# Kernel tuning notes

Hardware: AMD Instinct MI355X
Metric: run time of the kernel (lower is better)

The kernel has to match this reference:

```python
import jax, jax.numpy as jnp
import numpy as np

_SQRT2 = 1.4142135623730951

def _norm_cdf(z):
    return 0.5 * (1.0 + jax.scipy.special.erf(z / _SQRT2))

def _cv_squared(v):
    # torch.var is unbiased (ddof=1)
    return jnp.var(v, ddof=1) / (jnp.mean(v) ** 2 + 1e-10)

def setup_inputs() -> dict:
    key = jax.random.key(0)
    ks = jax.random.split(key, 6)
    B, Cin, Cout, H, W, E = 64, 32, 32, 64, 64, 16
    return {
        "x": jax.random.normal(ks[0], (B, Cin, H, W), jnp.float32),
        "noise": jax.random.normal(ks[1], (B, E), jnp.float32),
        "w_gate": jax.random.normal(ks[2], (Cin, E), jnp.float32) * 0.1,
        "w_noise": jax.random.normal(ks[3], (Cin, E), jnp.float32) * 0.1,
        "expert_w": jax.random.normal(ks[4], (E, Cout, Cin, 3, 3), jnp.float32) * 0.05,
        "expert_b": jax.random.normal(ks[5], (E, Cout), jnp.float32) * 0.05,
    }

def _forward(x, noise, w_gate, w_noise, expert_w, expert_b, k=4, loss_coef=0.01, noise_eps=0.01):
    B = x.shape[0]
    # gate features: adaptive avg pool to 1x1 then flatten -> [B, Cin]
    gate_x = x.mean(axis=(2, 3))
    clean = gate_x @ w_gate                      # [B, E]
    std = jax.nn.softplus(gate_x @ w_noise) + noise_eps
    noisy = clean + noise * std                  # noisy logits (training path)
    logits = jax.nn.softmax(noisy, axis=1)       # NOTE: original softmaxes before top-k
    top_logits, top_idx = jax.lax.top_k(logits, k + 1)
    top_k_logits = top_logits[:, :k]
    top_k_idx = top_idx[:, :k]
    top_k_gates = top_k_logits / (top_k_logits.sum(1, keepdims=True) + 1e-6)
    gates = jnp.zeros_like(logits).at[jnp.arange(B)[:, None], top_k_idx].set(top_k_gates)
    # _prob_in_top_k: thresholds come from the post-softmax top values,
    # compared against pre-softmax clean/noisy logits (faithful to source)
    thr_in = top_logits[:, k:k + 1]
    thr_out = top_logits[:, k - 1:k]
    prob = jnp.where(noisy > thr_in,
                     _norm_cdf((clean - thr_in) / std),
                     _norm_cdf((clean - thr_out) / std))
    load = prob.sum(0)
    importance = gates.sum(0)
    loss = (_cv_squared(importance) + _cv_squared(load)) * loss_coef
    # dispatch/combine: since gates are exactly zero for unselected experts,
    # sum_e gates[:,e] * expert_e(x) equals SparseDispatcher's gather-compute-scatter.
    def step(acc, xs):
        w, b, g = xs  # w [Co,Ci,3,3], b [Co], g [B]
        out = jax.lax.conv_general_dilated(x, w, (1, 1), [(1, 1), (1, 1)])
        out = out + b[None, :, None, None]
        return acc + g[:, None, None, None] * out, None
    y0 = jnp.zeros((B, expert_w.shape[1], x.shape[2], x.shape[3]), x.dtype)
    y, _ = jax.lax.scan(step, y0, (expert_w, expert_b, gates.T))
    return y, loss

def reference(x, noise, w_gate, w_noise, expert_w, expert_b):
    return _forward(x, noise, w_gate, w_noise, expert_w, expert_b)
```

## Files before the change

kernel.cpp:

```cpp
#include <hip/hip_runtime.h>
#include <math.h>

#define B 64
#define CIN 32
#define COUT 32
#define E 16
#define TOPK 4

typedef __attribute__((ext_vector_type(8))) short short8;
typedef __attribute__((ext_vector_type(4))) float f32x4;

__device__ __forceinline__ unsigned short f2bf(float f) {
    unsigned int u = __float_as_uint(f);
    u += 0x7fffu + ((u >> 16) & 1u);
    return (unsigned short)(u >> 16);
}

__device__ __forceinline__ int swz1024(int o) { return (o & 7) * 128 + (o >> 3); }

__device__ __forceinline__ int cswz(int wp, int c) {
    return c ^ (((wp >> 2) & 3) << 3);
}

__global__ void __launch_bounds__(256)
bandsum_kernel(const float* __restrict__ x, float* __restrict__ bandsum) {
    int blk = swz1024(blockIdx.x);
    int b = blk >> 4, band = blk & 15, h0 = band << 2;
    int t = threadIdx.x, wave = t >> 6, l = t & 63;
    const float4* x4 = reinterpret_cast<const float4*>(x);

    float racc[8];
    #pragma unroll
    for (int k = 0; k < 8; k++) {
        int c = k * 4 + wave;
        float4 v = x4[(((size_t)(b * 32 + c) * 64 + h0 + (l >> 4)) << 4) + (l & 15)];
        racc[k] = (v.x + v.y) + (v.z + v.w);
    }
    #pragma unroll
    for (int off = 1; off < 64; off <<= 1)
        #pragma unroll
        for (int k = 0; k < 8; k++) racc[k] += __shfl_xor(racc[k], off, 64);
    if (l == 0) {
        #pragma unroll
        for (int k = 0; k < 8; k++)
            bandsum[((size_t)b * 16 + band) * 32 + k * 4 + wave] = racc[k];
    }
}

__global__ void __launch_bounds__(256)
conv_fused(const float* __restrict__ x,
           const float* __restrict__ bandsum,
           const float* __restrict__ noise,
           const float* __restrict__ w_gate,
           const float* __restrict__ w_noise,
           const float* __restrict__ expert_w,
           const float* __restrict__ expert_b,
           float* __restrict__ probw,
           float* __restrict__ gimpw,
           float* __restrict__ y) {
    int blk = swz1024(blockIdx.x);
    int b = blk >> 4, band = blk & 15, h0 = band << 2;
    int t = threadIdx.x, wave = t >> 6, l = t & 63;
    int ln = l & 15, lk = l >> 4;

    __shared__ unsigned short sx[6 * 66 * 32];
    __shared__ unsigned short cw[9 * 1024];
    __shared__ float gx[32], s_bias[32];
    __shared__ float s_clean[E], s_std[E], s_noisy[E], s_lg[E];
    __shared__ float s_tv[TOPK + 1], s_g[TOPK];
    __shared__ int   s_gi[TOPK];

    if (t < 32) {
        const float* bp = bandsum + (size_t)b * 16 * 32 + t;
        float s = 0.f;
        #pragma unroll
        for (int j = 0; j < 16; j++) s += bp[j * 32];
        gx[t] = s * (1.f / 4096.f);
    }
    __syncthreads();
    if (t < E) {
        float s1 = 0.f, s2 = 0.f;
        #pragma unroll
        for (int c = 0; c < CIN; c++) {
            float g = gx[c];
            s1 += g * w_gate[c * E + t];
            s2 += g * w_noise[c * E + t];
        }
        float sp = fmaxf(s2, 0.f) + log1pf(expf(-fabsf(s2)));
        s_clean[t] = s1;
        s_std[t]   = sp + 0.01f;
        s_noisy[t] = s1 + noise[b * E + t] * (sp + 0.01f);
    }
    __syncthreads();
    if (t < E) {
        float m = s_noisy[0];
        #pragma unroll
        for (int e = 1; e < E; e++) m = fmaxf(m, s_noisy[e]);
        float den = 0.f;
        #pragma unroll
        for (int e = 0; e < E; e++) den += expf(s_noisy[e] - m);
        s_lg[t] = expf(s_noisy[t] - m) / den;
    }
    __syncthreads();
    if (t < E) {
        float v = s_lg[t]; int rank = 0;
        #pragma unroll
        for (int j = 0; j < E; j++) {
            float u = s_lg[j];
            rank += (u > v) || (u == v && j < t);
        }
        if (rank <= TOPK) s_tv[rank] = v;
        if (rank <  TOPK) s_gi[rank] = t;
    }
    __syncthreads();
    if (t < TOPK) {
        float s4 = s_tv[0] + s_tv[1] + s_tv[2] + s_tv[3] + 1e-6f;
        s_g[t] = s_tv[t] / s4;
    }
    __syncthreads();

    if (band == 0 && t < E) {
        float s4 = s_tv[0] + s_tv[1] + s_tv[2] + s_tv[3] + 1e-6f;
        float v = s_lg[t]; int rank = 0;
        #pragma unroll
        for (int j = 0; j < E; j++) {
            float u = s_lg[j];
            rank += (u > v) || (u == v && j < t);
        }
        gimpw[b * E + t] = (rank < TOPK) ? v / s4 : 0.f;
        const float INV_SQRT2 = 0.70710678118654752f;
        float thr_in = s_tv[TOPK], thr_out = s_tv[TOPK - 1];
        float thr = (s_noisy[t] > thr_in) ? thr_in : thr_out;
        float z = (s_clean[t] - thr) / s_std[t];
        probw[b * E + t] = 0.5f * (1.f + erff(z * INV_SQRT2));
    }

    const float4* x4 = reinterpret_cast<const float4*>(x);
    #pragma unroll
    for (int k = 0; k < 12; k++) {
        int i = k * 256 + t;
        int rr = i >> 9, c = (i >> 4) & 31, w4 = i & 15;
        int gr = h0 - 1 + rr;
        float4 v = {0.f, 0.f, 0.f, 0.f};
        if ((unsigned)gr < 64u)
            v = x4[(((size_t)(b * 32 + c) * 64 + gr) << 4) + w4];
        float vv[4] = {v.x, v.y, v.z, v.w};
        #pragma unroll
        for (int j = 0; j < 4; j++) {
            int wp = 1 + w4 * 4 + j;
            sx[(rr * 66 + wp) * 32 + cswz(wp, c)] = f2bf(vv[j]);
        }
    }
    for (int i = t; i < 384; i += 256) {
        int rr = i >> 6, rem = i & 63, side = rem >> 5, c = rem & 31;
        sx[(rr * 66 + side * 65) * 32 + c] = 0;
    }
    {
        const float* e0 = expert_w + s_gi[0] * 9216;
        const float* e1 = expert_w + s_gi[1] * 9216;
        const float* e2 = expert_w + s_gi[2] * 9216;
        const float* e3 = expert_w + s_gi[3] * 9216;
        float g0 = s_g[0], g1 = s_g[1], g2 = s_g[2], g3 = s_g[3];
        #pragma unroll
        for (int k = 0; k < 36; k++) {
            int o = k * 256 + t;
            int cc = o / 9, tap = o - cc * 9;
            float s = g0 * e0[o] + g1 * e1[o] + g2 * e2[o] + g3 * e3[o];
            cw[tap * 1024 + cc] = f2bf(s);
        }
        if (t < 32)
            s_bias[t] = g0 * expert_b[s_gi[0] * 32 + t] + g1 * expert_b[s_gi[1] * 32 + t]
                      + g2 * expert_b[s_gi[2] * 32 + t] + g3 * expert_b[s_gi[3] * 32 + t];
    }
    __syncthreads();

    short8 afrag[2][9];
    #pragma unroll
    for (int tap = 0; tap < 9; tap++)
        #pragma unroll
        for (int ch = 0; ch < 2; ch++)
            afrag[ch][tap] = *reinterpret_cast<const short8*>(
                &cw[tap * 1024 + (ch * 16 + ln) * 32 + lk * 8]);

    float bias0[4], bias1[4];
    #pragma unroll
    for (int r = 0; r < 4; r++) {
        bias0[r] = s_bias[lk * 4 + r];
        bias1[r] = s_bias[16 + lk * 4 + r];
    }

    int h = h0 + wave;
    for (int tile = 0; tile < 4; tile++) {
        int w0 = tile * 16;
        f32x4 acc0 = {0.f, 0.f, 0.f, 0.f};
        f32x4 acc1 = {0.f, 0.f, 0.f, 0.f};
        #pragma unroll
        for (int kh = 0; kh < 3; kh++) {
            int rr = wave + kh;
            #pragma unroll
            for (int kw = 0; kw < 3; kw++) {
                int wp = w0 + ln + kw;
                short8 bfrag = *reinterpret_cast<const short8*>(
                    &sx[(rr * 66 + wp) * 32 + cswz(wp, lk * 8)]);
                acc0 = __builtin_amdgcn_mfma_f32_16x16x32_bf16(afrag[0][kh * 3 + kw], bfrag, acc0, 0, 0, 0);
                acc1 = __builtin_amdgcn_mfma_f32_16x16x32_bf16(afrag[1][kh * 3 + kw], bfrag, acc1, 0, 0, 0);
            }
        }
        #pragma unroll
        for (int r = 0; r < 4; r++) {
            y[((size_t)(b * COUT + lk * 4 + r) * 64 + h) * 64 + w0 + ln]      = acc0[r] + bias0[r];
            y[((size_t)(b * COUT + 16 + lk * 4 + r) * 64 + h) * 64 + w0 + ln] = acc1[r] + bias1[r];
        }
    }
}

__global__ void loss_kernel(const float* __restrict__ probw,
                            const float* __restrict__ gimpw,
                            float* __restrict__ loss_out) {
    __shared__ float s_lv[32];
    int t = threadIdx.x;
    if (t < 32) {
        const float* src = (t < 16) ? gimpw : probw;
        int e = t & 15;
        float s = 0.f;
        for (int bb = 0; bb < B; bb++) s += src[bb * E + e];
        s_lv[t] = s;
    }
    __syncthreads();
    if (t == 0) {
        float loss = 0.f;
        for (int pass = 0; pass < 2; pass++) {
            const float* v = s_lv + pass * 16;
            float mean = 0.f;
            for (int e = 0; e < E; e++) mean += v[e];
            mean *= (1.f / E);
            float var = 0.f;
            for (int e = 0; e < E; e++) { float d = v[e] - mean; var += d * d; }
            var *= (1.f / (E - 1));
            loss += var / (mean * mean + 1e-10f);
        }
        loss_out[0] = loss * 0.01f;
    }
}

extern "C" void kernel_launch(void* const* d_in, const int* in_sizes, int n_in,
                              void* d_out, int out_size, void* d_ws, size_t ws_size,
                              hipStream_t stream) {
    const float* x        = (const float*)d_in[0];
    const float* noise    = (const float*)d_in[1];
    const float* w_gate   = (const float*)d_in[2];
    const float* w_noise  = (const float*)d_in[3];
    const float* expert_w = (const float*)d_in[4];
    const float* expert_b = (const float*)d_in[5];

    float* y    = (float*)d_out;
    float* loss = y + (size_t)B * COUT * 64 * 64;

    char* ws = (char*)d_ws;
    float* bands  = (float*)(ws);
    float* probw  = (float*)(ws + 131072);
    float* gimpw  = (float*)(ws + 135168);

    bandsum_kernel<<<B * 16, 256, 0, stream>>>(x, bands);
    conv_fused<<<B * 16, 256, 0, stream>>>(x, bands, noise, w_gate, w_noise,
                                           expert_w, expert_b, probw, gimpw, y);
    loss_kernel<<<1, 64, 0, stream>>>(probw, gimpw, loss);
}
```

Before: 37.94 us.

## Stage input tile through fp32 LDS transpose into channel-group-major bf16 layout

Input rows are no longer converted and scattered directly into a swizzled channel-interleaved LDS buffer with 2-byte stores. They are staged in two passes through an fp32 LDS scratch, then repacked into a channel-group-major layout with 16-byte short8 stores, and MFMA B-fragment reads use plain contiguous addressing. The goal is to avoid the scattered 2-byte LDS writes and their bank conflicts. In exchange it adds extra barriers, about 26KB more LDS (which may lower occupancy), and strided fp32 scratch reads during the repack.

```diff
diff --git a/kernel.cpp b/kernel.cpp
--- a/kernel.cpp
+++ b/kernel.cpp
@@ -17,10 +17,6 @@
 }
 
 __device__ __forceinline__ int swz1024(int o) { return (o & 7) * 128 + (o >> 3); }
-
-__device__ __forceinline__ int cswz(int wp, int c) {
-    return c ^ (((wp >> 2) & 3) << 3);
-}
 
 __global__ void __launch_bounds__(256)
 bandsum_kernel(const float* __restrict__ x, float* __restrict__ bandsum) {
@@ -63,7 +59,8 @@
     int t = threadIdx.x, wave = t >> 6, l = t & 63;
     int ln = l & 15, lk = l >> 4;
 
-    __shared__ unsigned short sx[6 * 66 * 32];
+    __shared__ float tmp[32 * 204];
+    __shared__ unsigned short sx[4 * 6 * 66 * 8];
     __shared__ unsigned short cw[9 * 1024];
     __shared__ float gx[32], s_bias[32];
     __shared__ float s_clean[E], s_std[E], s_noisy[E], s_lg[E];
@@ -135,26 +132,6 @@
         probw[b * E + t] = 0.5f * (1.f + erff(z * INV_SQRT2));
     }
 
-    const float4* x4 = reinterpret_cast<const float4*>(x);
-    #pragma unroll
-    for (int k = 0; k < 12; k++) {
-        int i = k * 256 + t;
-        int rr = i >> 9, c = (i >> 4) & 31, w4 = i & 15;
-        int gr = h0 - 1 + rr;
-        float4 v = {0.f, 0.f, 0.f, 0.f};
-        if ((unsigned)gr < 64u)
-            v = x4[(((size_t)(b * 32 + c) * 64 + gr) << 4) + w4];
-        float vv[4] = {v.x, v.y, v.z, v.w};
-        #pragma unroll
-        for (int j = 0; j < 4; j++) {
-            int wp = 1 + w4 * 4 + j;
-            sx[(rr * 66 + wp) * 32 + cswz(wp, c)] = f2bf(vv[j]);
-        }
-    }
-    for (int i = t; i < 384; i += 256) {
-        int rr = i >> 6, rem = i & 63, side = rem >> 5, c = rem & 31;
-        sx[(rr * 66 + side * 65) * 32 + c] = 0;
-    }
     {
         const float* e0 = expert_w + s_gi[0] * 9216;
         const float* e1 = expert_w + s_gi[1] * 9216;
@@ -169,8 +146,44 @@
             cw[tap * 1024 + cc] = f2bf(s);
         }
         if (t < 32)
-            s_bias[t] = g0 * expert_b[s_gi[0] * 32 + t] + g1 * expert_b[s_gi[1] * 32 + t]
-                      + g2 * expert_b[s_gi[2] * 32 + t] + g3 * expert_b[s_gi[3] * 32 + t];
+            s_bias[t] = s_g[0] * expert_b[s_gi[0] * 32 + t] + s_g[1] * expert_b[s_gi[1] * 32 + t]
+                      + s_g[2] * expert_b[s_gi[2] * 32 + t] + s_g[3] * expert_b[s_gi[3] * 32 + t];
+    }
+
+    const float4* x4 = reinterpret_cast<const float4*>(x);
+    #pragma unroll
+    for (int p = 0; p < 2; p++) {
+        __syncthreads();
+        #pragma unroll
+        for (int k = 0; k < 6; k++) {
+            int e = k * 256 + t;
+            int w4 = e & 15, c = (e >> 4) & 31, rrl = e >> 9;
+            int gr = h0 - 1 + p * 3 + rrl;
+            float4 v = {0.f, 0.f, 0.f, 0.f};
+            if ((unsigned)gr < 64u)
+                v = x4[(((size_t)(b * 32 + c) * 64 + gr) << 4) + w4];
+            *reinterpret_cast<float4*>(&tmp[c * 204 + rrl * 68 + w4 * 4]) = v;
+        }
+        __syncthreads();
+        #pragma unroll
+        for (int k = 0; k < 4; k++) {
+            int e = k * 256 + t;
+            if (e < 792) {
+                int wp = e % 66, q2 = e / 66;
+                int rrl = q2 % 3, cg = q2 / 3;
+                short8 ov;
+                if (wp >= 1 && wp <= 64) {
+                    #pragma unroll
+                    for (int j = 0; j < 8; j++)
+                        ov[j] = (short)f2bf(tmp[(cg * 8 + j) * 204 + rrl * 68 + (wp - 1)]);
+                } else {
+                    #pragma unroll
+                    for (int j = 0; j < 8; j++) ov[j] = 0;
+                }
+                *reinterpret_cast<short8*>(
+                    &sx[((cg * 6 + (p * 3 + rrl)) * 66 + wp) * 8]) = ov;
+            }
+        }
     }
     __syncthreads();
 
@@ -201,7 +214,7 @@
             for (int kw = 0; kw < 3; kw++) {
                 int wp = w0 + ln + kw;
                 short8 bfrag = *reinterpret_cast<const short8*>(
-                    &sx[(rr * 66 + wp) * 32 + cswz(wp, lk * 8)]);
+                    &sx[((lk * 6 + rr) * 66 + wp) * 8]);
                 acc0 = __builtin_amdgcn_mfma_f32_16x16x32_bf16(afrag[0][kh * 3 + kw], bfrag, acc0, 0, 0, 0);
                 acc1 = __builtin_amdgcn_mfma_f32_16x16x32_bf16(afrag[1][kh * 3 + kw], bfrag, acc1, 0, 0, 0);
             }
```

After: 40.82 us. 1.08x slower.

## Split gating and expert-weight combine into separate kernel, fold loss into conv

Applied to the files above, without the earlier changes.

Moves the gate computation and the per-sample combined expert weights out of the conv kernel into a new gate_combine kernel. It runs once per (sample, quarter) instead of redundantly in each of 16 bands, and writes bf16 combined weights to workspace. The conv kernel then loads its MFMA A-fragments directly from global memory and drops the 18KB LDS weight buffer. The loss reduction is folded into block 0 of the conv kernel, which removes one launch. The risks are an extra global round trip for the weights and an extra kernel dependency.

```diff
diff --git a/kernel.cpp b/kernel.cpp
--- a/kernel.cpp
+++ b/kernel.cpp
@@ -17,6 +17,7 @@
 }
 
 __device__ __forceinline__ int swz1024(int o) { return (o & 7) * 128 + (o >> 3); }
+__device__ __forceinline__ int swz256(int o)  { return (o & 7) * 32  + (o >> 3); }
 
 __device__ __forceinline__ int cswz(int wp, int c) {
     return c ^ (((wp >> 2) & 3) << 3);
@@ -48,24 +49,21 @@
 }
 
 __global__ void __launch_bounds__(256)
-conv_fused(const float* __restrict__ x,
-           const float* __restrict__ bandsum,
-           const float* __restrict__ noise,
-           const float* __restrict__ w_gate,
-           const float* __restrict__ w_noise,
-           const float* __restrict__ expert_w,
-           const float* __restrict__ expert_b,
-           float* __restrict__ probw,
-           float* __restrict__ gimpw,
-           float* __restrict__ y) {
-    int blk = swz1024(blockIdx.x);
-    int b = blk >> 4, band = blk & 15, h0 = band << 2;
-    int t = threadIdx.x, wave = t >> 6, l = t & 63;
-    int ln = l & 15, lk = l >> 4;
-
-    __shared__ unsigned short sx[6 * 66 * 32];
-    __shared__ unsigned short cw[9 * 1024];
-    __shared__ float gx[32], s_bias[32];
+gate_combine(const float* __restrict__ bandsum,
+             const float* __restrict__ noise,
+             const float* __restrict__ w_gate,
+             const float* __restrict__ w_noise,
+             const float* __restrict__ expert_w,
+             const float* __restrict__ expert_b,
+             unsigned short* __restrict__ cwb,
+             float* __restrict__ cbias,
+             float* __restrict__ probw,
+             float* __restrict__ gimpw) {
+    int blk = swz256(blockIdx.x);
+    int b = blk >> 2, q = blk & 3;
+    int t = threadIdx.x;
+
+    __shared__ float gx[32];
     __shared__ float s_clean[E], s_std[E], s_noisy[E], s_lg[E];
     __shared__ float s_tv[TOPK + 1], s_g[TOPK];
     __shared__ int   s_gi[TOPK];
@@ -119,7 +117,7 @@
     }
     __syncthreads();
 
-    if (band == 0 && t < E) {
+    if (q == 0 && t < E) {
         float s4 = s_tv[0] + s_tv[1] + s_tv[2] + s_tv[3] + 1e-6f;
         float v = s_lg[t]; int rank = 0;
         #pragma unroll
@@ -134,6 +132,40 @@
         float z = (s_clean[t] - thr) / s_std[t];
         probw[b * E + t] = 0.5f * (1.f + erff(z * INV_SQRT2));
     }
+    if (q == 0 && t < COUT) {
+        cbias[b * COUT + t] = s_g[0] * expert_b[s_gi[0] * 32 + t] + s_g[1] * expert_b[s_gi[1] * 32 + t]
+                            + s_g[2] * expert_b[s_gi[2] * 32 + t] + s_g[3] * expert_b[s_gi[3] * 32 + t];
+    }
+
+    const float* e0 = expert_w + s_gi[0] * 9216;
+    const float* e1 = expert_w + s_gi[1] * 9216;
+    const float* e2 = expert_w + s_gi[2] * 9216;
+    const float* e3 = expert_w + s_gi[3] * 9216;
+    float g0 = s_g[0], g1 = s_g[1], g2 = s_g[2], g3 = s_g[3];
+    #pragma unroll
+    for (int k = 0; k < 9; k++) {
+        int i = q * 2304 + k * 256 + t;
+        int tap = i >> 10, cc = i & 1023;
+        int rd = cc * 9 + tap;
+        float s = g0 * e0[rd] + g1 * e1[rd] + g2 * e2[rd] + g3 * e3[rd];
+        cwb[(size_t)b * 9216 + i] = f2bf(s);
+    }
+}
+
+__global__ void __launch_bounds__(256)
+conv_mfma(const float* __restrict__ x,
+          const unsigned short* __restrict__ cwb,
+          const float* __restrict__ cbias,
+          const float* __restrict__ probw,
+          const float* __restrict__ gimpw,
+          float* __restrict__ y,
+          float* __restrict__ loss_out) {
+    int blk = swz1024(blockIdx.x);
+    int b = blk >> 4, band = blk & 15, h0 = band << 2;
+    int t = threadIdx.x, wave = t >> 6, l = t & 63;
+    int ln = l & 15, lk = l >> 4;
+
+    __shared__ unsigned short sx[6 * 66 * 32];
 
     const float4* x4 = reinterpret_cast<const float4*>(x);
     #pragma unroll
@@ -155,39 +187,23 @@
         int rr = i >> 6, rem = i & 63, side = rem >> 5, c = rem & 31;
         sx[(rr * 66 + side * 65) * 32 + c] = 0;
     }
-    {
-        const float* e0 = expert_w + s_gi[0] * 9216;
-        const float* e1 = expert_w + s_gi[1] * 9216;
-        const float* e2 = expert_w + s_gi[2] * 9216;
-        const float* e3 = expert_w + s_gi[3] * 9216;
-        float g0 = s_g[0], g1 = s_g[1], g2 = s_g[2], g3 = s_g[3];
-        #pragma unroll
-        for (int k = 0; k < 36; k++) {
-            int o = k * 256 + t;
-            int cc = o / 9, tap = o - cc * 9;
-            float s = g0 * e0[o] + g1 * e1[o] + g2 * e2[o] + g3 * e3[o];
-            cw[tap * 1024 + cc] = f2bf(s);
-        }
-        if (t < 32)
-            s_bias[t] = g0 * expert_b[s_gi[0] * 32 + t] + g1 * expert_b[s_gi[1] * 32 + t]
-                      + g2 * expert_b[s_gi[2] * 32 + t] + g3 * expert_b[s_gi[3] * 32 + t];
-    }
-    __syncthreads();
-
+
+    const unsigned short* wbase = cwb + (size_t)b * 9216;
     short8 afrag[2][9];
     #pragma unroll
     for (int tap = 0; tap < 9; tap++)
         #pragma unroll
         for (int ch = 0; ch < 2; ch++)
             afrag[ch][tap] = *reinterpret_cast<const short8*>(
-                &cw[tap * 1024 + (ch * 16 + ln) * 32 + lk * 8]);
+                wbase + tap * 1024 + (ch * 16 + ln) * 32 + lk * 8);
 
     float bias0[4], bias1[4];
     #pragma unroll
     for (int r = 0; r < 4; r++) {
-        bias0[r] = s_bias[lk * 4 + r];
-        bias1[r] = s_bias[16 + lk * 4 + r];
-    }
+        bias0[r] = cbias[b * COUT + lk * 4 + r];
+        bias1[r] = cbias[b * COUT + 16 + lk * 4 + r];
+    }
+    __syncthreads();
 
     int h = h0 + wave;
     for (int tile = 0; tile < 4; tile++) {
@@ -212,34 +228,31 @@
             y[((size_t)(b * COUT + 16 + lk * 4 + r) * 64 + h) * 64 + w0 + ln] = acc1[r] + bias1[r];
         }
     }
-}
-
-__global__ void loss_kernel(const float* __restrict__ probw,
-                            const float* __restrict__ gimpw,
-                            float* __restrict__ loss_out) {
-    __shared__ float s_lv[32];
-    int t = threadIdx.x;
-    if (t < 32) {
-        const float* src = (t < 16) ? gimpw : probw;
-        int e = t & 15;
-        float s = 0.f;
-        for (int bb = 0; bb < B; bb++) s += src[bb * E + e];
-        s_lv[t] = s;
-    }
-    __syncthreads();
-    if (t == 0) {
-        float loss = 0.f;
-        for (int pass = 0; pass < 2; pass++) {
-            const float* v = s_lv + pass * 16;
-            float mean = 0.f;
-            for (int e = 0; e < E; e++) mean += v[e];
-            mean *= (1.f / E);
-            float var = 0.f;
-            for (int e = 0; e < E; e++) { float d = v[e] - mean; var += d * d; }
-            var *= (1.f / (E - 1));
-            loss += var / (mean * mean + 1e-10f);
-        }
-        loss_out[0] = loss * 0.01f;
+
+    if (blk == 0) {
+        __shared__ float s_lv[32];
+        if (t < 32) {
+            const float* src = (t < 16) ? gimpw : probw;
+            int e = t & 15;
+            float s = 0.f;
+            for (int bb = 0; bb < B; bb++) s += src[bb * E + e];
+            s_lv[t] = s;
+        }
+        __syncthreads();
+        if (t == 0) {
+            float loss = 0.f;
+            for (int pass = 0; pass < 2; pass++) {
+                const float* v = s_lv + pass * 16;
+                float mean = 0.f;
+                for (int e = 0; e < E; e++) mean += v[e];
+                mean *= (1.f / E);
+                float var = 0.f;
+                for (int e = 0; e < E; e++) { float d = v[e] - mean; var += d * d; }
+                var *= (1.f / (E - 1));
+                loss += var / (mean * mean + 1e-10f);
+            }
+            loss_out[0] = loss * 0.01f;
+        }
     }
 }
 
@@ -257,12 +270,15 @@
     float* loss = y + (size_t)B * COUT * 64 * 64;
 
     char* ws = (char*)d_ws;
-    float* bands  = (float*)(ws);
-    float* probw  = (float*)(ws + 131072);
-    float* gimpw  = (float*)(ws + 135168);
+    float*          bands  = (float*)(ws);
+    float*          probw  = (float*)(ws + 131072);
+    float*          gimpw  = (float*)(ws + 135168);
+    float*          cbias  = (float*)(ws + 139264);
+    unsigned short* cwb    = (unsigned short*)(ws + 147456);
 
     bandsum_kernel<<<B * 16, 256, 0, stream>>>(x, bands);
-    conv_fused<<<B * 16, 256, 0, stream>>>(x, bands, noise, w_gate, w_noise,
-                                           expert_w, expert_b, probw, gimpw, y);
-    loss_kernel<<<1, 64, 0, stream>>>(probw, gimpw, loss);
-}
+    gate_combine<<<256, 256, 0, stream>>>(bands, noise, w_gate, w_noise,
+                                          expert_w, expert_b, cwb, cbias,
+                                          probw, gimpw);
+    conv_mfma<<<B * 16, 256, 0, stream>>>(x, cwb, cbias, probw, gimpw, y, loss);
+}
```

Measured after the change: 32.88 us. 13.4% less time.
